# Performance work log

Hardware: AMD Instinct MI355X
Metric: run time of the kernel (lower is better)

## Reference

```python
import jax, jax.numpy as jnp
import numpy as np

N_NODES = 50000
N_EDGES = 800000
IN_CH = 256
HID = 64
HEADS = 4
OUT_CH = 4
NEG_SLOPE = 0.2


def _add_self_loops(edge_index, n):
    ar = jnp.arange(n, dtype=edge_index.dtype)
    loops = jnp.stack([ar, ar])
    return jnp.concatenate([edge_index, loops], axis=1)


def _gat_conv(x, edge_index, W, att_src, att_dst, bias, heads, ch):
    # PyG GATConv (no edge features, add_self_loops=True, concat=True)
    n = x.shape[0]
    ei = _add_self_loops(edge_index, n)
    src, dst = ei[0], ei[1]
    xp = (x @ W).reshape(n, heads, ch)            # [N,H,C]
    a_src = (xp * att_src).sum(-1)                 # [N,H]
    a_dst = (xp * att_dst).sum(-1)                 # [N,H]
    alpha = jax.nn.leaky_relu(a_src[src] + a_dst[dst], NEG_SLOPE)  # [E',H]
    amax = jax.ops.segment_max(alpha, dst, num_segments=n)
    alpha = jnp.exp(alpha - amax[dst])
    denom = jax.ops.segment_sum(alpha, dst, num_segments=n)
    alpha = alpha / (denom[dst] + 1e-16)
    msg = xp[src] * alpha[:, :, None]              # [E',H,C]
    out = jax.ops.segment_sum(msg, dst, num_segments=n)  # [N,H,C]
    return out.reshape(n, heads * ch) + bias


def setup_inputs() -> dict:
    key = jax.random.key(0)
    ks = jax.random.split(key, 12)
    x = jax.random.normal(ks[0], (N_NODES, IN_CH), dtype=jnp.float32)
    edge_index = jax.random.randint(ks[1], (2, N_EDGES), 0, N_NODES, dtype=jnp.int64)
    w = jax.random.uniform(ks[2], (N_EDGES,), dtype=jnp.float32)
    s1 = 1.0 / np.sqrt(IN_CH)
    s2 = 1.0 / np.sqrt(HEADS * HID)
    return {
        "x": x, "edge_index": edge_index, "w": w,
        "W1": jax.random.normal(ks[3], (IN_CH, HEADS * HID), dtype=jnp.float32) * s1,
        "att_src1": jax.random.normal(ks[4], (1, HEADS, HID), dtype=jnp.float32) * s2,
        "att_dst1": jax.random.normal(ks[5], (1, HEADS, HID), dtype=jnp.float32) * s2,
        "b1": jnp.zeros((HEADS * HID,), dtype=jnp.float32),
        "W2": jax.random.normal(ks[6], (HEADS * HID, HID), dtype=jnp.float32) * s2,
        "att_src2": jax.random.normal(ks[7], (1, 1, HID), dtype=jnp.float32) * s2,
        "att_dst2": jax.random.normal(ks[8], (1, 1, HID), dtype=jnp.float32) * s2,
        "b2": jnp.zeros((HID,), dtype=jnp.float32),
        "Wc": jax.random.normal(ks[9], (2 * HID, OUT_CH), dtype=jnp.float32) * (1.0 / np.sqrt(2 * HID)),
        "bc": jnp.zeros((OUT_CH,), dtype=jnp.float32),
    }


def reference(x, edge_index, w, W1, att_src1, att_dst1, b1,
              W2, att_src2, att_dst2, b2, Wc, bc):
    # w (edge_attr) is ignored: GATConv was built without edge_dim, so no lin_edge.
    h = _gat_conv(x, edge_index, W1, att_src1, att_dst1, b1, HEADS, HID)
    h = jax.nn.relu(h)
    h = _gat_conv(h, edge_index, W2, att_src2, att_dst2, b2, 1, HID)
    row, col = edge_index[0], edge_index[1]
    edge_emb = jnp.concatenate([h[row], h[col]], axis=-1)  # [E, 2*HID]
    return edge_emb @ Wc + bc
```

## Files before the change

### kernel.cpp

```cpp
#include <hip/hip_runtime.h>


#define NEG 0.2f

typedef __attribute__((ext_vector_type(8))) short bf16x8;
typedef __attribute__((ext_vector_type(4))) float f32x4;

__device__ __forceinline__ unsigned short f2bf(float f) {
    unsigned int u = __float_as_uint(f);
    unsigned int r = (u + 0x7FFFu + ((u >> 16) & 1u)) >> 16;
    return (unsigned short)r;
}
__device__ __forceinline__ float bf2f(unsigned short h) {
    return __uint_as_float(((unsigned int)h) << 16);
}
__device__ __forceinline__ float bflo(unsigned int u) { return __uint_as_float(u << 16); }
__device__ __forceinline__ float bfhi(unsigned int u) { return __uint_as_float(u & 0xFFFF0000u); }
__device__ __forceinline__ float lrelu(float x) { return x > 0.f ? x : NEG * x; }

__device__ __forceinline__ void async16(const void* g, void* l) {
    __builtin_amdgcn_global_load_lds(
        (const __attribute__((address_space(1))) unsigned int*)g,
        (__attribute__((address_space(3))) unsigned int*)l, 16, 0, 0);
}


__global__ __launch_bounds__(256) void k_init(int* deg, int* cur, int n) {
    int i = blockIdx.x * 256 + threadIdx.x;
    if (i < n) { deg[i] = 1; cur[i] = 0; }
}

__global__ __launch_bounds__(256) void k_hist(const int* __restrict__ ei, int* deg, int E) {
    int e = blockIdx.x * 256 + threadIdx.x;
    if (e < E) atomicAdd(&deg[ei[E + e]], 1);
}

__global__ __launch_bounds__(256) void k_bsum(const int* __restrict__ deg, int* __restrict__ bsum, int n) {
    int i = blockIdx.x * 256 + threadIdx.x;
    int v = (i < n) ? deg[i] : 0;
#pragma unroll
    for (int off = 1; off < 64; off <<= 1) v += __shfl_xor(v, off, 64);
    __shared__ int ws[4];
    int wv = threadIdx.x >> 6, l = threadIdx.x & 63;
    if (l == 0) ws[wv] = v;
    __syncthreads();
    if (threadIdx.x == 0) bsum[blockIdx.x] = ws[0] + ws[1] + ws[2] + ws[3];
}

__global__ __launch_bounds__(256) void k_bscan(const int* __restrict__ bsum, int* __restrict__ boff,
                                               int* __restrict__ rowptr, int nb, int n) {
    __shared__ int s[256];
    int t = threadIdx.x;
    int v = (t < nb) ? bsum[t] : 0;
    s[t] = v;
    __syncthreads();
    for (int off = 1; off < 256; off <<= 1) {
        int u = (t >= off) ? s[t - off] : 0;
        __syncthreads();
        s[t] += u;
        __syncthreads();
    }
    if (t < nb) boff[t] = s[t] - v;
    if (t == nb - 1) rowptr[n] = s[t];
}

__global__ __launch_bounds__(256) void k_rowptr(const int* __restrict__ deg, const int* __restrict__ boff,
                                                int* __restrict__ rowptr, int n) {
    __shared__ int s[256];
    int i = blockIdx.x * 256 + threadIdx.x;
    int t = threadIdx.x;
    int v = (i < n) ? deg[i] : 0;
    s[t] = v;
    __syncthreads();
    for (int off = 1; off < 256; off <<= 1) {
        int u = (t >= off) ? s[t - off] : 0;
        __syncthreads();
        s[t] += u;
        __syncthreads();
    }
    if (i < n) rowptr[i] = boff[blockIdx.x] + s[t] - v;
}

__global__ __launch_bounds__(256) void k_scatter(const int* __restrict__ ei, const int* __restrict__ rowptr,
                                                 int* cur, int* csr_src, int E, int N) {
    int e = blockIdx.x * 256 + threadIdx.x;
    if (e < E) {
        int d = ei[E + e];
        int pos = rowptr[d] + atomicAdd(&cur[d], 1);
        csr_src[pos] = ei[e];
    } else if (e < E + N) {
        int i = e - E;
        int pos = rowptr[i] + atomicAdd(&cur[i], 1);
        csr_src[pos] = i;
    }
}


__global__ __launch_bounds__(256) void k_pack_split(const float* __restrict__ src,
                                                    unsigned short* __restrict__ hi,
                                                    unsigned short* __restrict__ lo, long n4) {
    long i = (long)blockIdx.x * 256 + threadIdx.x;
    long stride = (long)gridDim.x * 256;
    for (; i < n4; i += stride) {
        float4 v = ((const float4*)src)[i];
        unsigned short h0 = f2bf(v.x), h1 = f2bf(v.y), h2 = f2bf(v.z), h3 = f2bf(v.w);
        ushort4 H = make_ushort4(h0, h1, h2, h3);
        ushort4 L = make_ushort4(f2bf(v.x - bf2f(h0)), f2bf(v.y - bf2f(h1)),
                                 f2bf(v.z - bf2f(h2)), f2bf(v.w - bf2f(h3)));
        ((ushort4*)hi)[i] = H;
        ((ushort4*)lo)[i] = L;
    }
}

__global__ __launch_bounds__(256) void k_pack_wT(const float* __restrict__ W,
                                                 unsigned short* __restrict__ hiT,
                                                 unsigned short* __restrict__ loT, int K, int N) {
    int t = blockIdx.x * 256 + threadIdx.x;
    if (t >= K * N) return;
    int n = t / K, k = t - n * K;
    float v = W[(size_t)k * N + n];
    unsigned short h = f2bf(v);
    hiT[t] = h;
    loT[t] = f2bf(v - bf2f(h));
}

template<int WGM, int WGN>
__global__ __launch_bounds__(256, 2) void k_gemm_lds(const unsigned short* __restrict__ Ah,
                                                     const unsigned short* __restrict__ Al,
                                                     const unsigned short* __restrict__ BhT,
                                                     const unsigned short* __restrict__ BlT,
                                                     unsigned short* __restrict__ Cb, int M, int N, int K) {
    constexpr int BM = WGM * 64, BN = WGN * 64;
    __shared__ char lds[(BM + BN) * 256];
    char* LAh = lds;
    char* LAl = lds + BM * 128;
    char* LBh = lds + 2 * BM * 128;
    char* LBl = lds + 2 * BM * 128 + BN * 128;

    const int t = threadIdx.x, wv = t >> 6, l = t & 63;
    const int r = l & 15, hk = l >> 4;
    const int m0 = blockIdx.x * BM;
    const int n0 = blockIdx.y * BN;
    const int wr = wv / WGN, wc = wv % WGN;
    const int wrow0 = wr * 64, wcol0 = wc * 64;

    f32x4 acc[4][4];
#pragma unroll
    for (int i = 0; i < 4; i++)
#pragma unroll
        for (int j = 0; j < 4; j++) acc[i][j] = f32x4{0, 0, 0, 0};

    const int lrow8 = l >> 3;
    const int cbs = ((l & 7) ^ lrow8) << 4;
    const size_t K2 = (size_t)K * 2;
    const int NCH = K >> 6;

    for (int c = 0; c < NCH; ++c) {
        const int kk2 = c * 128;
        {
            const int SA = BM / 8;
            for (int i = wv; i < SA; i += 4) {
                int row = i * 8 + lrow8;
                size_t go = (size_t)(m0 + row) * K2 + kk2 + cbs;
                async16((const char*)Ah + go, LAh + i * 1024);
                async16((const char*)Al + go, LAl + i * 1024);
            }
            const int SB = BN / 8;
            for (int i = wv; i < SB; i += 4) {
                int row = i * 8 + lrow8;
                size_t go = (size_t)(n0 + row) * K2 + kk2 + cbs;
                async16((const char*)BhT + go, LBh + i * 1024);
                async16((const char*)BlT + go, LBl + i * 1024);
            }
        }
        __syncthreads();
#pragma unroll
        for (int ks = 0; ks < 2; ++ks) {
            const int cb = ks * 64 + hk * 16;
            bf16x8 a_h[4], a_l[4], b_h[4], b_l[4];
#pragma unroll
            for (int fm = 0; fm < 4; ++fm) {
                int row = wrow0 + fm * 16 + r;
                int ad = row * 128 + (cb ^ ((row & 7) << 4));
                a_h[fm] = *(const bf16x8*)(LAh + ad);
                a_l[fm] = *(const bf16x8*)(LAl + ad);
            }
#pragma unroll
            for (int fn = 0; fn < 4; ++fn) {
                int row = wcol0 + fn * 16 + r;
                int ad = row * 128 + (cb ^ ((row & 7) << 4));
                b_h[fn] = *(const bf16x8*)(LBh + ad);
                b_l[fn] = *(const bf16x8*)(LBl + ad);
            }
#pragma unroll
            for (int fm = 0; fm < 4; ++fm)
#pragma unroll
                for (int fn = 0; fn < 4; ++fn) {
                    acc[fm][fn] = __builtin_amdgcn_mfma_f32_16x16x32_bf16(a_h[fm], b_h[fn], acc[fm][fn], 0, 0, 0);
                    acc[fm][fn] = __builtin_amdgcn_mfma_f32_16x16x32_bf16(a_h[fm], b_l[fn], acc[fm][fn], 0, 0, 0);
                    acc[fm][fn] = __builtin_amdgcn_mfma_f32_16x16x32_bf16(a_l[fm], b_h[fn], acc[fm][fn], 0, 0, 0);
                }
        }
        if (c + 1 < NCH) __syncthreads();
    }

#pragma unroll
    for (int fm = 0; fm < 4; ++fm)
#pragma unroll
        for (int fn = 0; fn < 4; ++fn)
#pragma unroll
            for (int j = 0; j < 4; ++j) {
                int m = m0 + wrow0 + fm * 16 + hk * 4 + j;
                if (m < M) Cb[(size_t)m * N + n0 + wcol0 + fn * 16 + r] = f2bf(acc[fm][fn][j]);
            }
}


__global__ __launch_bounds__(256) void k_attn(const unsigned short* __restrict__ xpb,
                                              const float* __restrict__ att_s,
                                              const float* __restrict__ att_d,
                                              float* __restrict__ as, float* __restrict__ ad,
                                              int M, int H) {
    int idx = blockIdx.x * 256 + threadIdx.x;
    if (idx >= M * H) return;
    int n = idx / H, h = idx - n * H;
    const uint4* row = (const uint4*)(xpb + (size_t)n * (64 * H) + h * 64);
    const float* fs = att_s + h * 64;
    const float* fd = att_d + h * 64;
    float s = 0.f, d = 0.f;
#pragma unroll
    for (int j = 0; j < 8; j++) {
        uint4 v = row[j];
        unsigned int uu[4] = {v.x, v.y, v.z, v.w};
#pragma unroll
        for (int q = 0; q < 4; q++) {
            float lo = bflo(uu[q]);
            float hi = bfhi(uu[q]);
            int c = j * 8 + q * 2;
            s += lo * fs[c] + hi * fs[c + 1];
            d += lo * fd[c] + hi * fd[c + 1];
        }
    }
    as[idx] = s; ad[idx] = d;
}

__global__ __launch_bounds__(256) void k_gather1(const unsigned short* __restrict__ xpb,
                                                 const float* __restrict__ as, const float* __restrict__ ad,
                                                 const int* __restrict__ rowptr, const int* __restrict__ csr_src,
                                                 const float* __restrict__ b1,
                                                 unsigned short* __restrict__ h1h, unsigned short* __restrict__ h1l,
                                                 int M) {
    int wv = threadIdx.x >> 6, lane = threadIdx.x & 63;
    int n = blockIdx.x * 4 + wv;
    if (n >= M) return;
    int h = lane >> 4;
    float adv = ad[n * 4 + h];
    int start = rowptr[n], end = rowptr[n + 1];
    float acc0[4] = {0.f, 0.f, 0.f, 0.f}, acc1[4] = {0.f, 0.f, 0.f, 0.f};
    float den0 = 0.f, den1 = 0.f;
    int e = start;
    for (; e + 1 < end; e += 2) {
        int s0 = csr_src[e], s1 = csr_src[e + 1];
        uint2 v0 = *(const uint2*)(xpb + (size_t)s0 * 256 + lane * 4);
        uint2 v1 = *(const uint2*)(xpb + (size_t)s1 * 256 + lane * 4);
        float p0 = __expf(lrelu(as[s0 * 4 + h] + adv));
        float p1 = __expf(lrelu(as[s1 * 4 + h] + adv));
        den0 += p0; den1 += p1;
        acc0[0] += p0 * bflo(v0.x); acc0[1] += p0 * bfhi(v0.x);
        acc0[2] += p0 * bflo(v0.y); acc0[3] += p0 * bfhi(v0.y);
        acc1[0] += p1 * bflo(v1.x); acc1[1] += p1 * bfhi(v1.x);
        acc1[2] += p1 * bflo(v1.y); acc1[3] += p1 * bfhi(v1.y);
    }
    if (e < end) {
        int s0 = csr_src[e];
        uint2 v0 = *(const uint2*)(xpb + (size_t)s0 * 256 + lane * 4);
        float p0 = __expf(lrelu(as[s0 * 4 + h] + adv));
        den0 += p0;
        acc0[0] += p0 * bflo(v0.x); acc0[1] += p0 * bfhi(v0.x);
        acc0[2] += p0 * bflo(v0.y); acc0[3] += p0 * bfhi(v0.y);
    }
    float dinv = 1.f / (den0 + den1 + 1e-16f);
    const float4 bb = *(const float4*)(b1 + lane * 4);
    float o0 = fmaxf((acc0[0] + acc1[0]) * dinv + bb.x, 0.f);
    float o1 = fmaxf((acc0[1] + acc1[1]) * dinv + bb.y, 0.f);
    float o2 = fmaxf((acc0[2] + acc1[2]) * dinv + bb.z, 0.f);
    float o3 = fmaxf((acc0[3] + acc1[3]) * dinv + bb.w, 0.f);
    unsigned short q0 = f2bf(o0), q1 = f2bf(o1), q2 = f2bf(o2), q3 = f2bf(o3);
    uint2 H, L;
    H.x = (unsigned)q0 | ((unsigned)q1 << 16);
    H.y = (unsigned)q2 | ((unsigned)q3 << 16);
    L.x = (unsigned)f2bf(o0 - bf2f(q0)) | ((unsigned)f2bf(o1 - bf2f(q1)) << 16);
    L.y = (unsigned)f2bf(o2 - bf2f(q2)) | ((unsigned)f2bf(o3 - bf2f(q3)) << 16);
    *(uint2*)(h1h + (size_t)n * 256 + lane * 4) = H;
    *(uint2*)(h1l + (size_t)n * 256 + lane * 4) = L;
}

__global__ __launch_bounds__(256) void k_gather2(const unsigned short* __restrict__ xp2b,
                                                 const float* __restrict__ as, const float* __restrict__ ad,
                                                 const int* __restrict__ rowptr, const int* __restrict__ csr_src,
                                                 const float* __restrict__ b2, const float* __restrict__ Wc,
                                                 float* __restrict__ uv, int M) {
    int wv = threadIdx.x >> 6, lane = threadIdx.x & 63;
    int n = blockIdx.x * 4 + wv;
    if (n >= M) return;
    int g = lane >> 4, q = lane & 15;
    float adv = ad[n];
    int start = rowptr[n], end = rowptr[n + 1];
    float acc[4] = {0.f, 0.f, 0.f, 0.f};
    float den = 0.f;
    for (int e = start; e < end; e += 4) {
        int ee = e + g;
        bool ok = ee < end;
        int s = csr_src[ok ? ee : start];
        uint2 v = *(const uint2*)(xp2b + (size_t)s * 64 + q * 4);
        float pw = ok ? __expf(lrelu(as[s] + adv)) : 0.f;
        den += pw;
        acc[0] += pw * bflo(v.x); acc[1] += pw * bfhi(v.x);
        acc[2] += pw * bflo(v.y); acc[3] += pw * bfhi(v.y);
    }
#pragma unroll
    for (int j = 0; j < 4; j++) {
        acc[j] += __shfl_xor(acc[j], 16, 64);
        acc[j] += __shfl_xor(acc[j], 32, 64);
    }
    den += __shfl_xor(den, 16, 64);
    den += __shfl_xor(den, 32, 64);
    float dinv = 1.f / (den + 1e-16f);
    float pr[8] = {0.f, 0.f, 0.f, 0.f, 0.f, 0.f, 0.f, 0.f};
#pragma unroll
    for (int j = 0; j < 4; j++) {
        int c = q * 4 + j;
        float val = acc[j] * dinv + b2[c];
#pragma unroll
        for (int k = 0; k < 4; k++) {
            pr[k]     += val * Wc[c * 4 + k];
            pr[4 + k] += val * Wc[(64 + c) * 4 + k];
        }
    }
#pragma unroll
    for (int off = 1; off <= 8; off <<= 1)
#pragma unroll
        for (int j = 0; j < 8; j++) pr[j] += __shfl_xor(pr[j], off, 64);
    if (lane == 0) {
        float4* o = (float4*)(uv + (size_t)n * 8);
        o[0] = make_float4(pr[0], pr[1], pr[2], pr[3]);
        o[1] = make_float4(pr[4], pr[5], pr[6], pr[7]);
    }
}

__global__ __launch_bounds__(256) void k_classify(const int* __restrict__ ei, const float* __restrict__ uv,
                                                  const float* __restrict__ bc, float* __restrict__ out, int E) {
    int e = blockIdx.x * 256 + threadIdx.x;
    if (e >= E) return;
    int r = ei[e];
    int c = ei[E + e];
    float4 u = *(const float4*)(uv + (size_t)r * 8);
    float4 v = *(const float4*)(uv + (size_t)c * 8 + 4);
    float4 o;
    o.x = u.x + v.x + bc[0];
    o.y = u.y + v.y + bc[1];
    o.z = u.z + v.z + bc[2];
    o.w = u.w + v.w + bc[3];
    *(float4*)(out + (size_t)e * 4) = o;
}


extern "C" void kernel_launch(void* const* d_in, const int* in_sizes, int n_in,
                              void* d_out, int out_size, void* d_ws, size_t ws_size,
                              hipStream_t stream) {
    const float* x    = (const float*)d_in[0];
    const int*   ei   = (const int*)d_in[1];
    const float* W1   = (const float*)d_in[3];
    const float* atS1 = (const float*)d_in[4];
    const float* atD1 = (const float*)d_in[5];
    const float* b1   = (const float*)d_in[6];
    const float* W2   = (const float*)d_in[7];
    const float* atS2 = (const float*)d_in[8];
    const float* atD2 = (const float*)d_in[9];
    const float* b2   = (const float*)d_in[10];
    const float* Wc   = (const float*)d_in[11];
    const float* bc   = (const float*)d_in[12];
    float* out = (float*)d_out;

    const int Nn = in_sizes[0] / 256;
    const int E = in_sizes[1] / 2;
    const int Etot = E + Nn;
    const int NB = (Nn + 255) / 256;

    char* w = (char*)d_ws;
    size_t off = 0;
    auto alloc = [&](size_t b) { size_t o = off; off = (o + b + 255) & ~(size_t)255; return o; };
    size_t oXH  = alloc((size_t)Nn * 256 * 2);
    size_t oXL  = alloc((size_t)Nn * 256 * 2);
    size_t oXPB = alloc((size_t)Nn * 256 * 2);
    size_t oAS1 = alloc((size_t)Nn * 4 * 4);
    size_t oAD1 = alloc((size_t)Nn * 4 * 4);
    size_t oDEG = alloc((size_t)Nn * 4);
    size_t oCUR = alloc((size_t)Nn * 4);
    size_t oRP  = alloc((size_t)(Nn + 1) * 4);
    size_t oCSR = alloc((size_t)Etot * 4);
    size_t oW1H = alloc((size_t)256 * 256 * 2);
    size_t oW1L = alloc((size_t)256 * 256 * 2);
    size_t oW2H = alloc((size_t)256 * 64 * 2);
    size_t oW2L = alloc((size_t)256 * 64 * 2);
    size_t oBS  = alloc((size_t)NB * 4);
    size_t oBO  = alloc((size_t)NB * 4);
    (void)ws_size;

    unsigned short* xh   = (unsigned short*)(w + oXH);
    unsigned short* xl   = (unsigned short*)(w + oXL);
    unsigned short* h1h  = (unsigned short*)(w + oXH);
    unsigned short* h1l  = (unsigned short*)(w + oXL);
    unsigned short* xpb  = (unsigned short*)(w + oXPB);
    unsigned short* xp2b = (unsigned short*)(w + oXPB);
    float* uv  = (float*)(w + oXPB + (size_t)Nn * 64 * 2 + 256);
    uv = (float*)(((uintptr_t)uv + 255) & ~(uintptr_t)255);
    float* as1 = (float*)(w + oAS1);
    float* ad1 = (float*)(w + oAD1);
    float* as2 = (float*)(w + oAS1);
    float* ad2 = (float*)(w + oAD1);
    int* deg    = (int*)(w + oDEG);
    int* cur    = (int*)(w + oCUR);
    int* rowptr = (int*)(w + oRP);
    int* csr    = (int*)(w + oCSR);
    int* bsum   = (int*)(w + oBS);
    int* boff   = (int*)(w + oBO);
    unsigned short* W1hT = (unsigned short*)(w + oW1H);
    unsigned short* W1lT = (unsigned short*)(w + oW1L);
    unsigned short* W2hT = (unsigned short*)(w + oW2H);
    unsigned short* W2lT = (unsigned short*)(w + oW2L);

    k_init<<<NB, 256, 0, stream>>>(deg, cur, Nn);
    k_hist<<<(E + 255) / 256, 256, 0, stream>>>(ei, deg, E);
    k_bsum<<<NB, 256, 0, stream>>>(deg, bsum, Nn);
    k_bscan<<<1, 256, 0, stream>>>(bsum, boff, rowptr, NB, Nn);
    k_rowptr<<<NB, 256, 0, stream>>>(deg, boff, rowptr, Nn);
    k_scatter<<<(Etot + 255) / 256, 256, 0, stream>>>(ei, rowptr, cur, csr, E, Nn);

    k_pack_split<<<2048, 256, 0, stream>>>(x, xh, xl, (long)Nn * 64);
    k_pack_wT<<<(256 * 256 + 255) / 256, 256, 0, stream>>>(W1, W1hT, W1lT, 256, 256);
    k_pack_wT<<<(256 * 64 + 255) / 256, 256, 0, stream>>>(W2, W2hT, W2lT, 256, 64);

    {
        dim3 g((Nn + 127) / 128, 2);
        k_gemm_lds<2, 2><<<g, 256, 0, stream>>>(xh, xl, W1hT, W1lT, xpb, Nn, 256, 256);
    }
    k_attn<<<(Nn * 4 + 255) / 256, 256, 0, stream>>>(xpb, atS1, atD1, as1, ad1, Nn, 4);
    k_gather1<<<(Nn + 3) / 4, 256, 0, stream>>>(xpb, as1, ad1, rowptr, csr, b1, h1h, h1l, Nn);

    {
        dim3 g((Nn + 255) / 256, 1);
        k_gemm_lds<4, 1><<<g, 256, 0, stream>>>(h1h, h1l, W2hT, W2lT, xp2b, Nn, 64, 256);
    }
    k_attn<<<(Nn + 255) / 256, 256, 0, stream>>>(xp2b, atS2, atD2, as2, ad2, Nn, 1);
    k_gather2<<<(Nn + 3) / 4, 256, 0, stream>>>(xp2b, as2, ad2, rowptr, csr, b2, Wc, uv, Nn);

    k_classify<<<(E + 255) / 256, 256, 0, stream>>>(ei, uv, bc, out, E);
}
```

Baseline: 315.9 us.

## Drop activation lo-split, fuse attention logits into GEMM epilogue, unroll gather

Activations are now held only as a single bf16 hi part, so the A-side lo buffer, its loads and one of the three MFMAs per tile are removed, while the weights keep their hi/lo split. The separate attention-logit kernel is folded into the GEMM epilogue, where per-head dot products are reduced across lanes with shuffles. The layer-1 gather loop is unrolled to four edges per iteration. This cuts memory traffic, MFMA work and two launches, at the cost of lower precision in the activations and in the attention logits computed from fp32 accumulators.

```diff
diff --git a/kernel.cpp b/kernel.cpp
--- a/kernel.cpp
+++ b/kernel.cpp
@@ -96,19 +96,13 @@
 }
 
 
-__global__ __launch_bounds__(256) void k_pack_split(const float* __restrict__ src,
-                                                    unsigned short* __restrict__ hi,
-                                                    unsigned short* __restrict__ lo, long n4) {
+__global__ __launch_bounds__(256) void k_pack_hi(const float* __restrict__ src,
+                                                 unsigned short* __restrict__ hi, long n4) {
     long i = (long)blockIdx.x * 256 + threadIdx.x;
     long stride = (long)gridDim.x * 256;
     for (; i < n4; i += stride) {
         float4 v = ((const float4*)src)[i];
-        unsigned short h0 = f2bf(v.x), h1 = f2bf(v.y), h2 = f2bf(v.z), h3 = f2bf(v.w);
-        ushort4 H = make_ushort4(h0, h1, h2, h3);
-        ushort4 L = make_ushort4(f2bf(v.x - bf2f(h0)), f2bf(v.y - bf2f(h1)),
-                                 f2bf(v.z - bf2f(h2)), f2bf(v.w - bf2f(h3)));
-        ((ushort4*)hi)[i] = H;
-        ((ushort4*)lo)[i] = L;
+        ((ushort4*)hi)[i] = make_ushort4(f2bf(v.x), f2bf(v.y), f2bf(v.z), f2bf(v.w));
     }
 }
 
@@ -126,16 +120,17 @@
 
 template<int WGM, int WGN>
 __global__ __launch_bounds__(256, 2) void k_gemm_lds(const unsigned short* __restrict__ Ah,
-                                                     const unsigned short* __restrict__ Al,
                                                      const unsigned short* __restrict__ BhT,
                                                      const unsigned short* __restrict__ BlT,
-                                                     unsigned short* __restrict__ Cb, int M, int N, int K) {
+                                                     unsigned short* __restrict__ Cb, int M, int N, int K,
+                                                     const float* __restrict__ att_s,
+                                                     const float* __restrict__ att_d,
+                                                     float* __restrict__ as, float* __restrict__ ad, int H) {
     constexpr int BM = WGM * 64, BN = WGN * 64;
-    __shared__ char lds[(BM + BN) * 256];
+    __shared__ char lds[BM * 128 + BN * 256];
     char* LAh = lds;
-    char* LAl = lds + BM * 128;
-    char* LBh = lds + 2 * BM * 128;
-    char* LBl = lds + 2 * BM * 128 + BN * 128;
+    char* LBh = lds + BM * 128;
+    char* LBl = lds + BM * 128 + BN * 128;
 
     const int t = threadIdx.x, wv = t >> 6, l = t & 63;
     const int r = l & 15, hk = l >> 4;
@@ -163,7 +158,6 @@
                 int row = i * 8 + lrow8;
                 size_t go = (size_t)(m0 + row) * K2 + kk2 + cbs;
                 async16((const char*)Ah + go, LAh + i * 1024);
-                async16((const char*)Al + go, LAl + i * 1024);
             }
             const int SB = BN / 8;
             for (int i = wv; i < SB; i += 4) {
@@ -177,20 +171,19 @@
 #pragma unroll
         for (int ks = 0; ks < 2; ++ks) {
             const int cb = ks * 64 + hk * 16;
-            bf16x8 a_h[4], a_l[4], b_h[4], b_l[4];
+            bf16x8 a_h[4], b_h[4], b_l[4];
 #pragma unroll
             for (int fm = 0; fm < 4; ++fm) {
                 int row = wrow0 + fm * 16 + r;
-                int ad = row * 128 + (cb ^ ((row & 7) << 4));
-                a_h[fm] = *(const bf16x8*)(LAh + ad);
-                a_l[fm] = *(const bf16x8*)(LAl + ad);
+                int ad_ = row * 128 + (cb ^ ((row & 7) << 4));
+                a_h[fm] = *(const bf16x8*)(LAh + ad_);
             }
 #pragma unroll
             for (int fn = 0; fn < 4; ++fn) {
                 int row = wcol0 + fn * 16 + r;
-                int ad = row * 128 + (cb ^ ((row & 7) << 4));
-                b_h[fn] = *(const bf16x8*)(LBh + ad);
-                b_l[fn] = *(const bf16x8*)(LBl + ad);
+                int ad_ = row * 128 + (cb ^ ((row & 7) << 4));
+                b_h[fn] = *(const bf16x8*)(LBh + ad_);
+                b_l[fn] = *(const bf16x8*)(LBl + ad_);
             }
 #pragma unroll
             for (int fm = 0; fm < 4; ++fm)
@@ -198,7 +191,6 @@
                 for (int fn = 0; fn < 4; ++fn) {
                     acc[fm][fn] = __builtin_amdgcn_mfma_f32_16x16x32_bf16(a_h[fm], b_h[fn], acc[fm][fn], 0, 0, 0);
                     acc[fm][fn] = __builtin_amdgcn_mfma_f32_16x16x32_bf16(a_h[fm], b_l[fn], acc[fm][fn], 0, 0, 0);
-                    acc[fm][fn] = __builtin_amdgcn_mfma_f32_16x16x32_bf16(a_l[fm], b_h[fn], acc[fm][fn], 0, 0, 0);
                 }
         }
         if (c + 1 < NCH) __syncthreads();
@@ -213,86 +205,92 @@
                 int m = m0 + wrow0 + fm * 16 + hk * 4 + j;
                 if (m < M) Cb[(size_t)m * N + n0 + wcol0 + fn * 16 + r] = f2bf(acc[fm][fn][j]);
             }
-}
-
-
-__global__ __launch_bounds__(256) void k_attn(const unsigned short* __restrict__ xpb,
-                                              const float* __restrict__ att_s,
-                                              const float* __restrict__ att_d,
-                                              float* __restrict__ as, float* __restrict__ ad,
-                                              int M, int H) {
-    int idx = blockIdx.x * 256 + threadIdx.x;
-    if (idx >= M * H) return;
-    int n = idx / H, h = idx - n * H;
-    const uint4* row = (const uint4*)(xpb + (size_t)n * (64 * H) + h * 64);
-    const float* fs = att_s + h * 64;
-    const float* fd = att_d + h * 64;
-    float s = 0.f, d = 0.f;
-#pragma unroll
-    for (int j = 0; j < 8; j++) {
-        uint4 v = row[j];
-        unsigned int uu[4] = {v.x, v.y, v.z, v.w};
-#pragma unroll
-        for (int q = 0; q < 4; q++) {
-            float lo = bflo(uu[q]);
-            float hi = bfhi(uu[q]);
-            int c = j * 8 + q * 2;
-            s += lo * fs[c] + hi * fs[c + 1];
-            d += lo * fd[c] + hi * fd[c + 1];
+
+    {
+        int head = (n0 + wcol0) >> 6;
+        float satt[4], datt[4];
+#pragma unroll
+        for (int fn = 0; fn < 4; ++fn) {
+            satt[fn] = att_s[head * 64 + fn * 16 + r];
+            datt[fn] = att_d[head * 64 + fn * 16 + r];
         }
-    }
-    as[idx] = s; ad[idx] = d;
-}
+#pragma unroll
+        for (int fm = 0; fm < 4; ++fm)
+#pragma unroll
+            for (int j = 0; j < 4; ++j) {
+                float ps = 0.f, pd = 0.f;
+#pragma unroll
+                for (int fn = 0; fn < 4; ++fn) {
+                    ps += satt[fn] * acc[fm][fn][j];
+                    pd += datt[fn] * acc[fm][fn][j];
+                }
+#pragma unroll
+                for (int off = 1; off <= 8; off <<= 1) {
+                    ps += __shfl_xor(ps, off, 64);
+                    pd += __shfl_xor(pd, off, 64);
+                }
+                if (r == 0) {
+                    int m = m0 + wrow0 + fm * 16 + hk * 4 + j;
+                    if (m < M) { as[m * H + head] = ps; ad[m * H + head] = pd; }
+                }
+            }
+    }
+}
+
 
 __global__ __launch_bounds__(256) void k_gather1(const unsigned short* __restrict__ xpb,
                                                  const float* __restrict__ as, const float* __restrict__ ad,
                                                  const int* __restrict__ rowptr, const int* __restrict__ csr_src,
                                                  const float* __restrict__ b1,
-                                                 unsigned short* __restrict__ h1h, unsigned short* __restrict__ h1l,
-                                                 int M) {
+                                                 unsigned short* __restrict__ h1h, int M) {
     int wv = threadIdx.x >> 6, lane = threadIdx.x & 63;
     int n = blockIdx.x * 4 + wv;
     if (n >= M) return;
     int h = lane >> 4;
     float adv = ad[n * 4 + h];
     int start = rowptr[n], end = rowptr[n + 1];
-    float acc0[4] = {0.f, 0.f, 0.f, 0.f}, acc1[4] = {0.f, 0.f, 0.f, 0.f};
+    float a0[4] = {0.f, 0.f, 0.f, 0.f}, a1[4] = {0.f, 0.f, 0.f, 0.f};
     float den0 = 0.f, den1 = 0.f;
     int e = start;
-    for (; e + 1 < end; e += 2) {
-        int s0 = csr_src[e], s1 = csr_src[e + 1];
+    for (; e + 3 < end; e += 4) {
+        int s0 = csr_src[e], s1 = csr_src[e + 1], s2 = csr_src[e + 2], s3 = csr_src[e + 3];
         uint2 v0 = *(const uint2*)(xpb + (size_t)s0 * 256 + lane * 4);
         uint2 v1 = *(const uint2*)(xpb + (size_t)s1 * 256 + lane * 4);
-        float p0 = __expf(lrelu(as[s0 * 4 + h] + adv));
-        float p1 = __expf(lrelu(as[s1 * 4 + h] + adv));
-        den0 += p0; den1 += p1;
-        acc0[0] += p0 * bflo(v0.x); acc0[1] += p0 * bfhi(v0.x);
-        acc0[2] += p0 * bflo(v0.y); acc0[3] += p0 * bfhi(v0.y);
-        acc1[0] += p1 * bflo(v1.x); acc1[1] += p1 * bfhi(v1.x);
-        acc1[2] += p1 * bflo(v1.y); acc1[3] += p1 * bfhi(v1.y);
-    }
-    if (e < end) {
+        uint2 v2 = *(const uint2*)(xpb + (size_t)s2 * 256 + lane * 4);
+        uint2 v3 = *(const uint2*)(xpb + (size_t)s3 * 256 + lane * 4);
+        float w0 = as[s0 * 4 + h], w1 = as[s1 * 4 + h], w2 = as[s2 * 4 + h], w3 = as[s3 * 4 + h];
+        float p0 = __expf(lrelu(w0 + adv));
+        float p1 = __expf(lrelu(w1 + adv));
+        float p2 = __expf(lrelu(w2 + adv));
+        float p3 = __expf(lrelu(w3 + adv));
+        den0 += p0 + p2; den1 += p1 + p3;
+        a0[0] += p0 * bflo(v0.x); a0[1] += p0 * bfhi(v0.x);
+        a0[2] += p0 * bflo(v0.y); a0[3] += p0 * bfhi(v0.y);
+        a1[0] += p1 * bflo(v1.x); a1[1] += p1 * bfhi(v1.x);
+        a1[2] += p1 * bflo(v1.y); a1[3] += p1 * bfhi(v1.y);
+        a0[0] += p2 * bflo(v2.x); a0[1] += p2 * bfhi(v2.x);
+        a0[2] += p2 * bflo(v2.y); a0[3] += p2 * bfhi(v2.y);
+        a1[0] += p3 * bflo(v3.x); a1[1] += p3 * bfhi(v3.x);
+        a1[2] += p3 * bflo(v3.y); a1[3] += p3 * bfhi(v3.y);
+    }
+    for (; e < end; ++e) {
         int s0 = csr_src[e];
         uint2 v0 = *(const uint2*)(xpb + (size_t)s0 * 256 + lane * 4);
         float p0 = __expf(lrelu(as[s0 * 4 + h] + adv));
         den0 += p0;
-        acc0[0] += p0 * bflo(v0.x); acc0[1] += p0 * bfhi(v0.x);
-        acc0[2] += p0 * bflo(v0.y); acc0[3] += p0 * bfhi(v0.y);
+        a0[0] += p0 * bflo(v0.x); a0[1] += p0 * bfhi(v0.x);
+        a0[2] += p0 * bflo(v0.y); a0[3] += p0 * bfhi(v0.y);
     }
     float dinv = 1.f / (den0 + den1 + 1e-16f);
     const float4 bb = *(const float4*)(b1 + lane * 4);
-    float o0 = fmaxf((acc0[0] + acc1[0]) * dinv + bb.x, 0.f);
-    float o1 = fmaxf((acc0[1] + acc1[1]) * dinv + bb.y, 0.f);
-    float o2 = fmaxf((acc0[2] + acc1[2]) * dinv + bb.z, 0.f);
-    float o3 = fmaxf((acc0[3] + acc1[3]) * dinv + bb.w, 0.f);
-    unsigned short q0 = f2bf(o0), q1 = f2bf(o1), q2 = f2bf(o2), q3 = f2bf(o3);
-    uint2 H, L;
-    H.x = (unsigned)q0 | ((unsigned)q1 << 16);
-    H.y = (unsigned)q2 | ((unsigned)q3 << 16);
-    L.x = (unsigned)f2bf(o0 - bf2f(q0)) | ((unsigned)f2bf(o1 - bf2f(q1)) << 16);
-    L.y = (unsigned)f2bf(o2 - bf2f(q2)) | ((unsigned)f2bf(o3 - bf2f(q3)) << 16);
+    float o0 = fmaxf((a0[0] + a1[0]) * dinv + bb.x, 0.f);
+    float o1 = fmaxf((a0[1] + a1[1]) * dinv + bb.y, 0.f);
+    float o2 = fmaxf((a0[2] + a1[2]) * dinv + bb.z, 0.f);
+    float o3 = fmaxf((a0[3] + a1[3]) * dinv + bb.w, 0.f);
+    uint2 H;
+    H.x = (unsigned)f2bf(o0) | ((unsigned)f2bf(o1) << 16);
+    H.y = (unsigned)f2bf(o2) | ((unsigned)f2bf(o3) << 16);
     *(uint2*)(h1h + (size_t)n * 256 + lane * 4) = H;
-    *(uint2*)(h1l + (size_t)n * 256 + lane * 4) = L;
 }
 
 __global__ __launch_bounds__(256) void k_gather2(const unsigned short* __restrict__ xp2b,
@@ -391,7 +389,6 @@
     size_t off = 0;
     auto alloc = [&](size_t b) { size_t o = off; off = (o + b + 255) & ~(size_t)255; return o; };
     size_t oXH  = alloc((size_t)Nn * 256 * 2);
-    size_t oXL  = alloc((size_t)Nn * 256 * 2);
     size_t oXPB = alloc((size_t)Nn * 256 * 2);
     size_t oAS1 = alloc((size_t)Nn * 4 * 4);
     size_t oAD1 = alloc((size_t)Nn * 4 * 4);
@@ -408,9 +405,7 @@
     (void)ws_size;
 
     unsigned short* xh   = (unsigned short*)(w + oXH);
-    unsigned short* xl   = (unsigned short*)(w + oXL);
     unsigned short* h1h  = (unsigned short*)(w + oXH);
-    unsigned short* h1l  = (unsigned short*)(w + oXL);
     unsigned short* xpb  = (unsigned short*)(w + oXPB);
     unsigned short* xp2b = (unsigned short*)(w + oXPB);
     float* uv  = (float*)(w + oXPB + (size_t)Nn * 64 * 2 + 256);
@@ -437,22 +432,22 @@
     k_rowptr<<<NB, 256, 0, stream>>>(deg, boff, rowptr, Nn);
     k_scatter<<<(Etot + 255) / 256, 256, 0, stream>>>(ei, rowptr, cur, csr, E, Nn);
 
-    k_pack_split<<<2048, 256, 0, stream>>>(x, xh, xl, (long)Nn * 64);
+    k_pack_hi<<<2048, 256, 0, stream>>>(x, xh, (long)Nn * 64);
     k_pack_wT<<<(256 * 256 + 255) / 256, 256, 0, stream>>>(W1, W1hT, W1lT, 256, 256);
     k_pack_wT<<<(256 * 64 + 255) / 256, 256, 0, stream>>>(W2, W2hT, W2lT, 256, 64);
 
     {
         dim3 g((Nn + 127) / 128, 2);
-        k_gemm_lds<2, 2><<<g, 256, 0, stream>>>(xh, xl, W1hT, W1lT, xpb, Nn, 256, 256);
-    }
-    k_attn<<<(Nn * 4 + 255) / 256, 256, 0, stream>>>(xpb, atS1, atD1, as1, ad1, Nn, 4);
-    k_gather1<<<(Nn + 3) / 4, 256, 0, stream>>>(xpb, as1, ad1, rowptr, csr, b1, h1h, h1l, Nn);
+        k_gemm_lds<2, 2><<<g, 256, 0, stream>>>(xh, W1hT, W1lT, xpb, Nn, 256, 256,
+                                                atS1, atD1, as1, ad1, 4);
+    }
+    k_gather1<<<(Nn + 3) / 4, 256, 0, stream>>>(xpb, as1, ad1, rowptr, csr, b1, h1h, Nn);
 
     {
         dim3 g((Nn + 255) / 256, 1);
-        k_gemm_lds<4, 1><<<g, 256, 0, stream>>>(h1h, h1l, W2hT, W2lT, xp2b, Nn, 64, 256);
-    }
-    k_attn<<<(Nn + 255) / 256, 256, 0, stream>>>(xp2b, atS2, atD2, as2, ad2, Nn, 1);
+        k_gemm_lds<4, 1><<<g, 256, 0, stream>>>(h1h, W2hT, W2lT, xp2b, Nn, 64, 256,
+                                                atS2, atD2, as2, ad2, 1);
+    }
     k_gather2<<<(Nn + 3) / 4, 256, 0, stream>>>(xp2b, as2, ad2, rowptr, csr, b2, Wc, uv, Nn);
 
     k_classify<<<(E + 255) / 256, 256, 0, stream>>>(ei, uv, bc, out, E);
```

Result: faster. 285.7 us (-9.6%).
